# Kernel optimization log

Hardware: AMD Instinct MI355X
Metric: run time of the kernel (lower is better)

Reference implementation:

```python
import jax, jax.numpy as jnp
import numpy as np
from jax import lax

T, D, NH, CATS = 1024, 2048, 2048, 1000


def setup_inputs() -> dict:
    key = jax.random.key(0)
    ks = jax.random.split(key, 16)
    s = 0.02
    return {
        "x": jax.random.normal(ks[0], (T, D), dtype=jnp.float32),
        "Wh": jax.random.normal(ks[1], (NH, D), dtype=jnp.float32) * s,
        "Wz": jax.random.normal(ks[2], (NH, D), dtype=jnp.float32) * s,
        "Wr": jax.random.normal(ks[3], (NH, D), dtype=jnp.float32) * s,
        "Uh": jax.random.normal(ks[4], (NH, NH), dtype=jnp.float32) * s,
        "Uz": jax.random.normal(ks[5], (NH, NH), dtype=jnp.float32) * s,
        "bz": jax.random.normal(ks[6], (NH,), dtype=jnp.float32) * s,
        "Ur": jax.random.normal(ks[7], (NH, NH), dtype=jnp.float32) * s,
        "br": jax.random.normal(ks[8], (NH,), dtype=jnp.float32) * s,
        "Wout": jax.random.normal(ks[9], (CATS, NH), dtype=jnp.float32) * s,
        "h0": jax.random.normal(ks[10], (NH,), dtype=jnp.float32),
        "zt0": jax.random.normal(ks[11], (NH,), dtype=jnp.float32),
        "htilde0": jax.random.normal(ks[12], (NH,), dtype=jnp.float32),
        "hprev0": jax.random.normal(ks[13], (NH,), dtype=jnp.float32),
    }


def reference(x, Wh, Wz, Wr, Uh, Uz, bz, Ur, br, Wout, h0, zt0, htilde0, hprev0):
    # Batch the input projections over all timesteps: [T,d] @ [d,nh] -> [T,nh]
    xh = x @ Wh.T
    xz = x @ Wz.T
    xr = x @ Wr.T

    # Faithful to the original update ORDER: h is computed from the *stale*
    # zt/htilde (from the previous iteration), then gates are refreshed.
    # The original's hadamard(a, b) = linear(a, diag(b)) is exactly a * b.
    def step(carry, xs):
        h, zt, htilde, hprev = carry
        xh_t, xz_t, xr_t = xs
        h_new = (1.0 - zt) * hprev + zt * htilde
        zt_new = jax.nn.sigmoid(xz_t + hprev @ Uz.T + bz)
        htilde_new = jnp.tanh(xh_t + hprev @ Uh.T)
        # rt = sigmoid(xr_t + hprev @ Ur.T + br)  # computed in original, never used
        return (h_new, zt_new, htilde_new, h_new), None

    (h_fin, _, _, _), _ = lax.scan(step, (h0, zt0, htilde0, hprev0), (xh, xz, xr))
    logits = h_fin @ Wout.T  # [cats]
    return jax.nn.softmax(logits, axis=0)
```

## Files before the change

kernel.cpp:

```cpp
#include <hip/hip_runtime.h>
#include <math.h>

#define TT  1024
#define DD  2048
#define NHH 2048
#define CC  1000

__global__ void k_init(unsigned long long* __restrict__ Hbuf) {
    int i = blockIdx.x * blockDim.x + threadIdx.x;
    if (i < 4 * NHH) Hbuf[i] = 0xFFFFFFFF00000000ull;
}

__global__ __launch_bounds__(256) void k_gemm(const float* __restrict__ X,
                                              const float* __restrict__ Wh,
                                              const float* __restrict__ Wz,
                                              const float* __restrict__ bz,
                                              float* __restrict__ XH,
                                              float* __restrict__ XZ) {
    __shared__ float As[32][68];
    __shared__ float Bs[32][68];
    const int z = blockIdx.z;
    const float* __restrict__ W = z ? Wz : Wh;
    float* __restrict__ OUT = z ? XZ : XH;
    const int n0 = blockIdx.x * 64;
    const int m0 = blockIdx.y * 64;
    const int tid = threadIdx.x;
    const int tx = tid & 15, ty = tid >> 4;
    const int lr = tid >> 2;
    const int lc = (tid & 3) * 8;

    float acc[4][4] = {};
    for (int k0 = 0; k0 < DD; k0 += 32) {
        float4 a0 = *(const float4*)&X[(size_t)(m0 + lr) * DD + k0 + lc];
        float4 a1 = *(const float4*)&X[(size_t)(m0 + lr) * DD + k0 + lc + 4];
        float4 b0 = *(const float4*)&W[(size_t)(n0 + lr) * DD + k0 + lc];
        float4 b1 = *(const float4*)&W[(size_t)(n0 + lr) * DD + k0 + lc + 4];
        As[lc+0][lr]=a0.x; As[lc+1][lr]=a0.y; As[lc+2][lr]=a0.z; As[lc+3][lr]=a0.w;
        As[lc+4][lr]=a1.x; As[lc+5][lr]=a1.y; As[lc+6][lr]=a1.z; As[lc+7][lr]=a1.w;
        Bs[lc+0][lr]=b0.x; Bs[lc+1][lr]=b0.y; Bs[lc+2][lr]=b0.z; Bs[lc+3][lr]=b0.w;
        Bs[lc+4][lr]=b1.x; Bs[lc+5][lr]=b1.y; Bs[lc+6][lr]=b1.z; Bs[lc+7][lr]=b1.w;
        __syncthreads();
#pragma unroll
        for (int kk = 0; kk < 32; ++kk) {
            float4 av = *(const float4*)&As[kk][ty * 4];
            float4 bv = *(const float4*)&Bs[kk][tx * 4];
            acc[0][0] = fmaf(av.x, bv.x, acc[0][0]); acc[0][1] = fmaf(av.x, bv.y, acc[0][1]);
            acc[0][2] = fmaf(av.x, bv.z, acc[0][2]); acc[0][3] = fmaf(av.x, bv.w, acc[0][3]);
            acc[1][0] = fmaf(av.y, bv.x, acc[1][0]); acc[1][1] = fmaf(av.y, bv.y, acc[1][1]);
            acc[1][2] = fmaf(av.y, bv.z, acc[1][2]); acc[1][3] = fmaf(av.y, bv.w, acc[1][3]);
            acc[2][0] = fmaf(av.z, bv.x, acc[2][0]); acc[2][1] = fmaf(av.z, bv.y, acc[2][1]);
            acc[2][2] = fmaf(av.z, bv.z, acc[2][2]); acc[2][3] = fmaf(av.z, bv.w, acc[2][3]);
            acc[3][0] = fmaf(av.w, bv.x, acc[3][0]); acc[3][1] = fmaf(av.w, bv.y, acc[3][1]);
            acc[3][2] = fmaf(av.w, bv.z, acc[3][2]); acc[3][3] = fmaf(av.w, bv.w, acc[3][3]);
        }
        __syncthreads();
    }
    float4 bias = make_float4(0.f, 0.f, 0.f, 0.f);
    if (z) bias = *(const float4*)&bz[n0 + tx * 4];
#pragma unroll
    for (int i = 0; i < 4; ++i) {
        float4 o = make_float4(acc[i][0] + bias.x, acc[i][1] + bias.y,
                               acc[i][2] + bias.z, acc[i][3] + bias.w);
        *(float4*)&OUT[(size_t)(m0 + ty * 4 + i) * NHH + n0 + tx * 4] = o;
    }
}

__global__ __launch_bounds__(256, 1) void k_recur(
    const float* __restrict__ XH, const float* __restrict__ XZ,
    const float* __restrict__ Uh, const float* __restrict__ Uz,
    const float* __restrict__ zt0, const float* __restrict__ ht0,
    const float* __restrict__ hp0,
    unsigned long long* __restrict__ Hbuf) {
    __shared__ float Us[16][NHH];
    __shared__ float Hs[NHH];
    __shared__ float dot_s[16];
    const int tid  = threadIdx.x;
    const int wave = tid >> 6, lane = tid & 63;
    const int base8 = blockIdx.x * 8;

#pragma unroll
    for (int r = 0; r < 8; ++r) {
        const float* __restrict__ gz = Uz + (size_t)(base8 + r) * NHH + tid * 8;
        const float* __restrict__ gh = Uh + (size_t)(base8 + r) * NHH + tid * 8;
        *(float4*)&Us[r][tid * 8]     = *(const float4*)&gz[0];
        *(float4*)&Us[r][tid * 8 + 4] = *(const float4*)&gz[4];
        *(float4*)&Us[8 + r][tid * 8]     = *(const float4*)&gh[0];
        *(float4*)&Us[8 + r][tid * 8 + 4] = *(const float4*)&gh[4];
    }

#pragma unroll
    for (int k = 0; k < 8; ++k) Hs[k * 256 + tid] = hp0[k * 256 + tid];

    float p_cur = 0.f;
    if (tid < 8) {
        float z0 = zt0[base8 + tid], g0 = ht0[base8 + tid], p0 = hp0[base8 + tid];
        p_cur = (1.0f - z0) * p0 + z0 * g0;
        unsigned long long pr = (1ull << 32) | (unsigned long long)__float_as_uint(p_cur);
        __hip_atomic_store(&Hbuf[(size_t)1 * NHH + base8 + tid], pr,
                           __ATOMIC_RELAXED, __HIP_MEMORY_SCOPE_AGENT);
    }
    __syncthreads();

    const int lr0 = (wave >> 1) * 8 + (wave & 1) * 4;
    const float* __restrict__ U0 = Us[lr0 + 0];
    const float* __restrict__ U1 = Us[lr0 + 1];
    const float* __restrict__ U2 = Us[lr0 + 2];
    const float* __restrict__ U3 = Us[lr0 + 3];

    for (int t = 1; t < TT; ++t) {
        const unsigned long long* __restrict__ src = Hbuf + (size_t)(t & 3) * NHH;
        unsigned long long pv[8];
#pragma unroll
        for (int k = 0; k < 8; ++k)
            pv[k] = __hip_atomic_load(&src[k * 256 + tid], __ATOMIC_RELAXED, __HIP_MEMORY_SCOPE_AGENT);
        float xzv = 0.f, xhv = 0.f;
        if (tid < 8) {
            xzv = XZ[(size_t)(t - 1) * NHH + base8 + tid];
            xhv = XH[(size_t)(t - 1) * NHH + base8 + tid];
        }
        float a0 = 0.f, a1 = 0.f, a2 = 0.f, a3 = 0.f;
#pragma unroll
        for (int c = 0; c < 8; ++c) {
            const int o = c * 256 + lane * 4;
            float4 h4 = *(const float4*)&Hs[o];
            float4 u0 = *(const float4*)&U0[o];
            float4 u1 = *(const float4*)&U1[o];
            float4 u2 = *(const float4*)&U2[o];
            float4 u3 = *(const float4*)&U3[o];
            a0 = fmaf(u0.x, h4.x, fmaf(u0.y, h4.y, fmaf(u0.z, h4.z, fmaf(u0.w, h4.w, a0))));
            a1 = fmaf(u1.x, h4.x, fmaf(u1.y, h4.y, fmaf(u1.z, h4.z, fmaf(u1.w, h4.w, a1))));
            a2 = fmaf(u2.x, h4.x, fmaf(u2.y, h4.y, fmaf(u2.z, h4.z, fmaf(u2.w, h4.w, a2))));
            a3 = fmaf(u3.x, h4.x, fmaf(u3.y, h4.y, fmaf(u3.z, h4.z, fmaf(u3.w, h4.w, a3))));
        }
#pragma unroll
        for (int off = 32; off > 0; off >>= 1) {
            a0 += __shfl_xor(a0, off);
            a1 += __shfl_xor(a1, off);
            a2 += __shfl_xor(a2, off);
            a3 += __shfl_xor(a3, off);
        }
        if (lane == 0) {
            int di = ((wave & 1) * 4) + ((wave >> 1) * 8);
            dot_s[di + 0] = a0; dot_s[di + 1] = a1; dot_s[di + 2] = a2; dot_s[di + 3] = a3;
        }
        __syncthreads();
        if (tid < 8) {
            float z = 1.0f / (1.0f + expf(-(xzv + dot_s[tid])));
            float g = tanhf(xhv + dot_s[8 + tid]);
            float pn = (1.0f - z) * p_cur + z * g;
            p_cur = pn;
            unsigned long long pr = ((unsigned long long)(unsigned)(t + 1) << 32)
                                  | (unsigned long long)__float_as_uint(pn);
            __hip_atomic_store(&Hbuf[(size_t)((t + 1) & 3) * NHH + base8 + tid], pr,
                               __ATOMIC_RELAXED, __HIP_MEMORY_SCOPE_AGENT);
        }
        for (;;) {
            unsigned stale = 0;
#pragma unroll
            for (int k = 0; k < 8; ++k)
                if ((unsigned)(pv[k] >> 32) != (unsigned)t) stale |= (1u << k);
            if (!stale) break;
#pragma unroll
            for (int k = 0; k < 8; ++k)
                if (stale & (1u << k))
                    pv[k] = __hip_atomic_load(&src[k * 256 + tid], __ATOMIC_RELAXED, __HIP_MEMORY_SCOPE_AGENT);
        }
#pragma unroll
        for (int k = 0; k < 8; ++k) Hs[k * 256 + tid] = __uint_as_float((unsigned)pv[k]);
        __syncthreads();
    }
}

__global__ __launch_bounds__(256) void k_logits(const unsigned long long* __restrict__ Hbuf,
                                                const float* __restrict__ Wout,
                                                float* __restrict__ lg) {
    __shared__ float Hs[NHH];
    const int tid = threadIdx.x;
    for (int k = tid; k < NHH; k += 256) Hs[k] = __uint_as_float((unsigned)Hbuf[k]);
    __syncthreads();
    const int wave = tid >> 6, lane = tid & 63;
    const int row = blockIdx.x * 4 + wave;
    float a = 0.f;
#pragma unroll
    for (int c = 0; c < 8; ++c) {
        float4 w = *(const float4*)&Wout[(size_t)row * NHH + c * 256 + lane * 4];
        float4 h = *(const float4*)&Hs[c * 256 + lane * 4];
        a = fmaf(w.x, h.x, fmaf(w.y, h.y, fmaf(w.z, h.z, fmaf(w.w, h.w, a))));
    }
#pragma unroll
    for (int off = 32; off > 0; off >>= 1) a += __shfl_xor(a, off);
    if (lane == 0) lg[row] = a;
}

__global__ __launch_bounds__(1024) void k_softmax(const float* __restrict__ lg,
                                                  float* __restrict__ out) {
    const int i = threadIdx.x;
    __shared__ float red[16];
    __shared__ float bc[2];
    float v = (i < CC) ? lg[i] : -3.0e38f;
    float m = v;
#pragma unroll
    for (int off = 32; off > 0; off >>= 1) m = fmaxf(m, __shfl_xor(m, off));
    if ((i & 63) == 0) red[i >> 6] = m;
    __syncthreads();
    if (i == 0) { float mm = red[0]; for (int k = 1; k < 16; ++k) mm = fmaxf(mm, red[k]); bc[0] = mm; }
    __syncthreads();
    float e = (i < CC) ? expf(v - bc[0]) : 0.f;
    float s = e;
#pragma unroll
    for (int off = 32; off > 0; off >>= 1) s += __shfl_xor(s, off);
    if ((i & 63) == 0) red[i >> 6] = s;
    __syncthreads();
    if (i == 0) { float ss = 0.f; for (int k = 0; k < 16; ++k) ss += red[k]; bc[1] = ss; }
    __syncthreads();
    if (i < CC) out[i] = e / bc[1];
}

extern "C" void kernel_launch(void* const* d_in, const int* in_sizes, int n_in,
                              void* d_out, int out_size, void* d_ws, size_t ws_size,
                              hipStream_t stream) {
    const float* x    = (const float*)d_in[0];
    const float* Wh   = (const float*)d_in[1];
    const float* Wz   = (const float*)d_in[2];
    const float* Uh   = (const float*)d_in[4];
    const float* Uz   = (const float*)d_in[5];
    const float* bz   = (const float*)d_in[6];
    const float* Wout = (const float*)d_in[9];
    const float* zt0  = (const float*)d_in[11];
    const float* ht0  = (const float*)d_in[12];
    const float* hp0  = (const float*)d_in[13];
    float* out = (float*)d_out;

    float* XH = (float*)d_ws;
    float* XZ = XH + (size_t)TT * NHH;
    unsigned long long* Hbuf = (unsigned long long*)(XZ + (size_t)TT * NHH);
    float* lg = (float*)(Hbuf + 4 * NHH);

    k_init<<<dim3((4 * NHH + 255) / 256), dim3(256), 0, stream>>>(Hbuf);
    k_gemm<<<dim3(NHH / 64, TT / 64, 2), dim3(256), 0, stream>>>(x, Wh, Wz, bz, XH, XZ);
    k_recur<<<dim3(256), dim3(256), 0, stream>>>(XH, XZ, Uh, Uz, zt0, ht0, hp0, Hbuf);
    k_logits<<<dim3(250), dim3(256), 0, stream>>>(Hbuf, Wout, lg);
    k_softmax<<<dim3(1), dim3(1024), 0, stream>>>(lg, out);
}
```

Baseline: 2.369 ms.

## Warp-specialize recurrence: split compute and global-poll waves with LDS double buffering

The recurrent kernel now runs 512 threads per block. Four waves compute the matvec and gate update, and four other waves poll the global Hbuf for the next hidden state and copy it into a double-buffered LDS H array. Workgroup-scope atomic counters replace __syncthreads as the handshake between the two groups, so the global poll latency can overlap with compute and the per-step barrier is removed. The XZ/XH values are also prefetched one step ahead. In exchange the kernel carries more spin-wait complexity, and 512-thread blocks with 2 blocks per CU requested may change occupancy and LDS pressure for the persistent grid.

```diff
diff --git a/kernel.cpp b/kernel.cpp
--- a/kernel.cpp
+++ b/kernel.cpp
@@ -5,6 +5,9 @@
 #define DD  2048
 #define NHH 2048
 #define CC  1000
+
+#define LDS_LOAD_ACQ(P)  __hip_atomic_load((P), __ATOMIC_ACQUIRE, __HIP_MEMORY_SCOPE_WORKGROUP)
+#define LDS_ADD_REL(P)   __hip_atomic_fetch_add((P), 1, __ATOMIC_RELEASE, __HIP_MEMORY_SCOPE_WORKGROUP)
 
 __global__ void k_init(unsigned long long* __restrict__ Hbuf) {
     int i = blockIdx.x * blockDim.x + threadIdx.x;
@@ -65,109 +68,124 @@
     }
 }
 
-__global__ __launch_bounds__(256, 1) void k_recur(
+__global__ __launch_bounds__(512, 2) void k_recur(
     const float* __restrict__ XH, const float* __restrict__ XZ,
     const float* __restrict__ Uh, const float* __restrict__ Uz,
     const float* __restrict__ zt0, const float* __restrict__ ht0,
     const float* __restrict__ hp0,
     unsigned long long* __restrict__ Hbuf) {
     __shared__ float Us[16][NHH];
-    __shared__ float Hs[NHH];
-    __shared__ float dot_s[16];
+    __shared__ float Hs[2][NHH];
+    __shared__ float dot_s[2][16];
+    __shared__ int mv_cnt, fill_cnt;
     const int tid  = threadIdx.x;
     const int wave = tid >> 6, lane = tid & 63;
     const int base8 = blockIdx.x * 8;
 
-#pragma unroll
-    for (int r = 0; r < 8; ++r) {
-        const float* __restrict__ gz = Uz + (size_t)(base8 + r) * NHH + tid * 8;
-        const float* __restrict__ gh = Uh + (size_t)(base8 + r) * NHH + tid * 8;
-        *(float4*)&Us[r][tid * 8]     = *(const float4*)&gz[0];
-        *(float4*)&Us[r][tid * 8 + 4] = *(const float4*)&gz[4];
-        *(float4*)&Us[8 + r][tid * 8]     = *(const float4*)&gh[0];
-        *(float4*)&Us[8 + r][tid * 8 + 4] = *(const float4*)&gh[4];
-    }
-
-#pragma unroll
-    for (int k = 0; k < 8; ++k) Hs[k * 256 + tid] = hp0[k * 256 + tid];
-
-    float p_cur = 0.f;
+    if (tid == 0) { mv_cnt = 0; fill_cnt = 0; }
+
+    {
+        const int c4 = tid * 4;
+#pragma unroll
+        for (int r = 0; r < 8; ++r) {
+            *(float4*)&Us[r][c4]     = *(const float4*)&Uz[(size_t)(base8 + r) * NHH + c4];
+            *(float4*)&Us[8 + r][c4] = *(const float4*)&Uh[(size_t)(base8 + r) * NHH + c4];
+        }
+    }
+    *(float4*)&Hs[0][tid * 4] = *(const float4*)&hp0[tid * 4];
+
+    float p_cur = 0.f, xz_cur = 0.f, xh_cur = 0.f;
     if (tid < 8) {
         float z0 = zt0[base8 + tid], g0 = ht0[base8 + tid], p0 = hp0[base8 + tid];
         p_cur = (1.0f - z0) * p0 + z0 * g0;
         unsigned long long pr = (1ull << 32) | (unsigned long long)__float_as_uint(p_cur);
         __hip_atomic_store(&Hbuf[(size_t)1 * NHH + base8 + tid], pr,
                            __ATOMIC_RELAXED, __HIP_MEMORY_SCOPE_AGENT);
-    }
-    __syncthreads();
-
-    const int lr0 = (wave >> 1) * 8 + (wave & 1) * 4;
-    const float* __restrict__ U0 = Us[lr0 + 0];
-    const float* __restrict__ U1 = Us[lr0 + 1];
-    const float* __restrict__ U2 = Us[lr0 + 2];
-    const float* __restrict__ U3 = Us[lr0 + 3];
-
-    for (int t = 1; t < TT; ++t) {
-        const unsigned long long* __restrict__ src = Hbuf + (size_t)(t & 3) * NHH;
-        unsigned long long pv[8];
-#pragma unroll
-        for (int k = 0; k < 8; ++k)
-            pv[k] = __hip_atomic_load(&src[k * 256 + tid], __ATOMIC_RELAXED, __HIP_MEMORY_SCOPE_AGENT);
-        float xzv = 0.f, xhv = 0.f;
-        if (tid < 8) {
-            xzv = XZ[(size_t)(t - 1) * NHH + base8 + tid];
-            xhv = XH[(size_t)(t - 1) * NHH + base8 + tid];
-        }
-        float a0 = 0.f, a1 = 0.f, a2 = 0.f, a3 = 0.f;
-#pragma unroll
-        for (int c = 0; c < 8; ++c) {
-            const int o = c * 256 + lane * 4;
-            float4 h4 = *(const float4*)&Hs[o];
-            float4 u0 = *(const float4*)&U0[o];
-            float4 u1 = *(const float4*)&U1[o];
-            float4 u2 = *(const float4*)&U2[o];
-            float4 u3 = *(const float4*)&U3[o];
-            a0 = fmaf(u0.x, h4.x, fmaf(u0.y, h4.y, fmaf(u0.z, h4.z, fmaf(u0.w, h4.w, a0))));
-            a1 = fmaf(u1.x, h4.x, fmaf(u1.y, h4.y, fmaf(u1.z, h4.z, fmaf(u1.w, h4.w, a1))));
-            a2 = fmaf(u2.x, h4.x, fmaf(u2.y, h4.y, fmaf(u2.z, h4.z, fmaf(u2.w, h4.w, a2))));
-            a3 = fmaf(u3.x, h4.x, fmaf(u3.y, h4.y, fmaf(u3.z, h4.z, fmaf(u3.w, h4.w, a3))));
-        }
-#pragma unroll
-        for (int off = 32; off > 0; off >>= 1) {
-            a0 += __shfl_xor(a0, off);
-            a1 += __shfl_xor(a1, off);
-            a2 += __shfl_xor(a2, off);
-            a3 += __shfl_xor(a3, off);
-        }
-        if (lane == 0) {
-            int di = ((wave & 1) * 4) + ((wave >> 1) * 8);
-            dot_s[di + 0] = a0; dot_s[di + 1] = a1; dot_s[di + 2] = a2; dot_s[di + 3] = a3;
-        }
-        __syncthreads();
-        if (tid < 8) {
-            float z = 1.0f / (1.0f + expf(-(xzv + dot_s[tid])));
-            float g = tanhf(xhv + dot_s[8 + tid]);
-            float pn = (1.0f - z) * p_cur + z * g;
-            p_cur = pn;
-            unsigned long long pr = ((unsigned long long)(unsigned)(t + 1) << 32)
-                                  | (unsigned long long)__float_as_uint(pn);
-            __hip_atomic_store(&Hbuf[(size_t)((t + 1) & 3) * NHH + base8 + tid], pr,
-                               __ATOMIC_RELAXED, __HIP_MEMORY_SCOPE_AGENT);
-        }
-        for (;;) {
-            unsigned stale = 0;
+        xz_cur = XZ[base8 + tid];
+        xh_cur = XH[base8 + tid];
+    }
+    __syncthreads();
+
+    if (wave < 4) {
+        const int lr0 = (wave >> 1) * 8 + (wave & 1) * 4;
+        const float* __restrict__ U0 = Us[lr0 + 0];
+        const float* __restrict__ U1 = Us[lr0 + 1];
+        const float* __restrict__ U2 = Us[lr0 + 2];
+        const float* __restrict__ U3 = Us[lr0 + 3];
+        const int di = ((wave & 1) * 4) + ((wave >> 1) * 8);
+
+        for (int t = 1; t < TT; ++t) {
+            if (t > 1)
+                while (LDS_LOAD_ACQ(&fill_cnt) < 4 * (t - 1)) __builtin_amdgcn_s_sleep(0);
+            const float* __restrict__ HA = Hs[(t - 1) & 1];
+            float a0 = 0.f, a1 = 0.f, a2 = 0.f, a3 = 0.f;
+#pragma unroll
+            for (int c = 0; c < 8; ++c) {
+                const int o = c * 256 + lane * 4;
+                float4 h4 = *(const float4*)&HA[o];
+                float4 u0 = *(const float4*)&U0[o];
+                float4 u1 = *(const float4*)&U1[o];
+                float4 u2 = *(const float4*)&U2[o];
+                float4 u3 = *(const float4*)&U3[o];
+                a0 = fmaf(u0.x, h4.x, fmaf(u0.y, h4.y, fmaf(u0.z, h4.z, fmaf(u0.w, h4.w, a0))));
+                a1 = fmaf(u1.x, h4.x, fmaf(u1.y, h4.y, fmaf(u1.z, h4.z, fmaf(u1.w, h4.w, a1))));
+                a2 = fmaf(u2.x, h4.x, fmaf(u2.y, h4.y, fmaf(u2.z, h4.z, fmaf(u2.w, h4.w, a2))));
+                a3 = fmaf(u3.x, h4.x, fmaf(u3.y, h4.y, fmaf(u3.z, h4.z, fmaf(u3.w, h4.w, a3))));
+            }
+#pragma unroll
+            for (int off = 32; off > 0; off >>= 1) {
+                a0 += __shfl_xor(a0, off);
+                a1 += __shfl_xor(a1, off);
+                a2 += __shfl_xor(a2, off);
+                a3 += __shfl_xor(a3, off);
+            }
+            if (lane == 0) {
+                float* dw = dot_s[t & 1];
+                dw[di + 0] = a0; dw[di + 1] = a1; dw[di + 2] = a2; dw[di + 3] = a3;
+                LDS_ADD_REL(&mv_cnt);
+            }
+            if (tid < 8) {
+                while (LDS_LOAD_ACQ(&mv_cnt) < 4 * t) __builtin_amdgcn_s_sleep(0);
+                const float* dr = dot_s[t & 1];
+                float z = 1.0f / (1.0f + expf(-(xz_cur + dr[tid])));
+                float g = tanhf(xh_cur + dr[8 + tid]);
+                p_cur = (1.0f - z) * p_cur + z * g;
+                unsigned long long pr = ((unsigned long long)(unsigned)(t + 1) << 32)
+                                      | (unsigned long long)__float_as_uint(p_cur);
+                __hip_atomic_store(&Hbuf[(size_t)((t + 1) & 3) * NHH + base8 + tid], pr,
+                                   __ATOMIC_RELAXED, __HIP_MEMORY_SCOPE_AGENT);
+                xz_cur = XZ[(size_t)t * NHH + base8 + tid];
+                xh_cur = XH[(size_t)t * NHH + base8 + tid];
+            }
+        }
+    } else {
+        const int ct = tid - 256;
+        for (int t = 1; t < TT; ++t) {
+            const unsigned long long* __restrict__ src = Hbuf + (size_t)(t & 3) * NHH;
+            unsigned long long pv[8];
 #pragma unroll
             for (int k = 0; k < 8; ++k)
-                if ((unsigned)(pv[k] >> 32) != (unsigned)t) stale |= (1u << k);
-            if (!stale) break;
+                pv[k] = __hip_atomic_load(&src[k * 256 + ct], __ATOMIC_RELAXED, __HIP_MEMORY_SCOPE_AGENT);
+            if (t > 1)
+                while (LDS_LOAD_ACQ(&mv_cnt) < 4 * (t - 1)) __builtin_amdgcn_s_sleep(0);
+            for (;;) {
+                unsigned stale = 0;
+#pragma unroll
+                for (int k = 0; k < 8; ++k)
+                    if ((unsigned)(pv[k] >> 32) != (unsigned)t) stale |= (1u << k);
+                if (!stale) break;
+                __builtin_amdgcn_s_sleep(1);
+#pragma unroll
+                for (int k = 0; k < 8; ++k)
+                    if (stale & (1u << k))
+                        pv[k] = __hip_atomic_load(&src[k * 256 + ct], __ATOMIC_RELAXED, __HIP_MEMORY_SCOPE_AGENT);
+            }
+            float* __restrict__ HB = Hs[t & 1];
 #pragma unroll
             for (int k = 0; k < 8; ++k)
-                if (stale & (1u << k))
-                    pv[k] = __hip_atomic_load(&src[k * 256 + tid], __ATOMIC_RELAXED, __HIP_MEMORY_SCOPE_AGENT);
-        }
-#pragma unroll
-        for (int k = 0; k < 8; ++k) Hs[k * 256 + tid] = __uint_as_float((unsigned)pv[k]);
-        __syncthreads();
+                HB[k * 256 + ct] = __uint_as_float((unsigned)pv[k]);
+            if (lane == 0) LDS_ADD_REL(&fill_cnt);
+        }
     }
 }
 
@@ -238,7 +256,7 @@
 
     k_init<<<dim3((4 * NHH + 255) / 256), dim3(256), 0, stream>>>(Hbuf);
     k_gemm<<<dim3(NHH / 64, TT / 64, 2), dim3(256), 0, stream>>>(x, Wh, Wz, bz, XH, XZ);
-    k_recur<<<dim3(256), dim3(256), 0, stream>>>(XH, XZ, Uh, Uz, zt0, ht0, hp0, Hbuf);
+    k_recur<<<dim3(256), dim3(512), 0, stream>>>(XH, XZ, Uh, Uz, zt0, ht0, hp0, Hbuf);
     k_logits<<<dim3(250), dim3(256), 0, stream>>>(Hbuf, Wout, lg);
     k_softmax<<<dim3(1), dim3(1024), 0, stream>>>(lg, out);
 }
```

Result: faster. 2.099 ms (-11.4%).
